# Kernel tuning notes

Hardware: AMD Instinct MI355X
Metric: run time of the kernel (lower is better)

The kernel has to match this reference:

```python
import jax, jax.numpy as jnp
import numpy as np

TAU = 0.1
K = 60.0
CHUNK = 64
B = 1024


def setup_inputs() -> dict:
    key = jax.random.key(0)
    k1, k2, k3, k4 = jax.random.split(key, 4)
    s_v = jax.random.normal(k1, (B, B), jnp.float32)
    s_l = jax.random.normal(k2, (B, B), jnp.float32)
    # class-label based positive/negative masks (typical metric-learning batch)
    labels = jax.random.randint(k3, (B,), 0, B // 8)
    pos_mask = labels[:, None] == labels[None, :]
    neg_mask = ~pos_mask
    w_v = jax.random.uniform(k4, (B, B), jnp.float32)
    w_l = 1.0 - w_v
    return dict(s_v=s_v, s_l=s_l, pos_mask=pos_mask, neg_mask=neg_mask, w_v=w_v, w_l=w_l)


def _soft_ranks(sim, pos_f, neg_f, tau=TAU, chunk=CHUNK):
    """Row-chunked differentiable soft ranks. sim/pos_f/neg_f: [B, B] float."""
    b = sim.shape[0]
    nc = b // chunk  # B divisible by chunk

    def body(args):
        cs, cp, cn = args                                   # [chunk, B] each
        # sig[c, k, j] = sigmoid((s_ck - s_cj) / tau)
        sig = jax.nn.sigmoid((cs[:, :, None] - cs[:, None, :]) / tau)
        rank_pos = 1.0 + jnp.einsum('ckj,ck->cj', sig, cn)  # count negatives above
        rank_neg = 1.0 + jnp.einsum('ckj,ck->cj', sig, cp)  # count positives above
        return rank_pos * cp + rank_neg * cn

    args = (sim.reshape(nc, chunk, b), pos_f.reshape(nc, chunk, b), neg_f.reshape(nc, chunk, b))
    return jax.lax.map(jax.checkpoint(body), args).reshape(b, b)


def reference(s_v, s_l, pos_mask, neg_mask, w_v, w_l):
    pos_f = pos_mask.astype(s_v.dtype)
    neg_f = neg_mask.astype(s_v.dtype)
    rank_v = _soft_ranks(s_v, pos_f, neg_f)
    rank_l = _soft_ranks(s_l, pos_f, neg_f)
    S_hat = (K + 1.0) * (w_v / (K + rank_v) + w_l / (K + rank_l))
    return S_hat
```

## Files before the change

### kernel.cpp

```cpp
#include <hip/hip_runtime.h>


#define NB 1024
#define CEXP 14.426950408889634f
#define SCL  0.000030517578125f
#define NBUK 86
#define BUK0 4.3f
#define BUKW 10.0f
#define DBUK 2
#define CHSZ 128
#define NJOB 32
#define MAXPOS 64

__device__ __forceinline__ float fma_sat(float a, float b, float c) {
    float d;
    asm("v_fma_f32 %0, %1, %2, %3 clamp" : "=v"(d) : "v"(a), "v"(b), "v"(c));
    return d;
}

__device__ __forceinline__ float nrcp(float d) {
    float r = __uint_as_float(0x7EF311C3u - __float_as_uint(d));
    r = r * fmaf(-d, r, 2.0f);
    return r;
}

#define TREE(Es, ra, rb, A)                                      \
    {                                                            \
        const float y1 = fma_sat((Es), (ra).x, SCL);             \
        const float y2 = fma_sat((Es), (ra).y, SCL);             \
        const float y3 = fma_sat((Es), (ra).z, SCL);             \
        const float y4 = fma_sat((Es), (ra).w, SCL);             \
        const float y5 = fma_sat((Es), (rb).x, SCL);             \
        const float y6 = fma_sat((Es), (rb).y, SCL);             \
        const float y7 = fma_sat((Es), (rb).z, SCL);             \
        const float y8 = fma_sat((Es), (rb).w, SCL);             \
        const float p12 = y1 * y2, p34 = y3 * y4;                \
        const float p56 = y5 * y6, p78 = y7 * y8;                \
        const float s12 = y1 + y2, s34 = y3 + y4;                \
        const float s56 = y5 + y6, s78 = y7 + y8;                \
        const float q1 = p12 * p34, q2 = p56 * p78;              \
        const float n1 = fmaf(s12, p34, s34 * p12);              \
        const float n2 = fmaf(s56, p78, s78 * p56);              \
        const float num = fmaf(n1, q2, n2 * q1);                 \
        const float den = q1 * q2;                               \
        (A) = fmaf(num, nrcp(den), (A));                         \
    }

__global__ __launch_bounds__(512) void drank_kernel(
    const float* __restrict__ s_v, const float* __restrict__ s_l,
    const unsigned char* __restrict__ pos_m,
    const unsigned char* __restrict__ neg_m,
    const float* __restrict__ w_v, const float* __restrict__ w_l,
    float* __restrict__ out)
{
    __shared__ float  listRv[NB], listRl[NB];
    __shared__ int    listJv[NB], listJl[NB];
    __shared__ float  sAv1[NB], sAl1[NB];
    __shared__ float  sAv2[NB], sAl2[NB];
    __shared__ int    offv[NBUK + 1], offl[NBUK + 1];
    __shared__ float  SRv[129], SEv[129];
    __shared__ float  SRl[129], SEl[129];
    __shared__ float2 posR[MAXPOS];
    __shared__ int    npos_s, jobCtr;

    int* curv = (int*)sAv1;
    int* curl = (int*)sAl1;

    const int c = blockIdx.x;
    const int t = threadIdx.x;
    const long row = (long)c * NB;

    if (t < NBUK) { curv[t] = 0; curl[t] = 0; }
    if (t == 0) { npos_s = 0; jobCtr = 0; }
    __syncthreads();

    const unsigned int W =
        ((const unsigned int*)pos_m)[0] ^ ((const unsigned int*)neg_m)[0];
    const int mode = (W == 0x01010101u) ? 0 : ((W == 0x3f800000u) ? 2 : 1);

    const int j0 = t * 2;
    const float2 sjv = *(const float2*)(s_v + row + j0);
    const float2 sjl = *(const float2*)(s_l + row + j0);
    const float svu[2] = {sjv.x, sjv.y};
    const float slu[2] = {sjl.x, sjl.y};

    float Rv[2], Rl[2], Ev[2], El[2];
    int ibv[2], ibl[2];
    #pragma unroll
    for (int u = 0; u < 2; ++u) {
        Rv[u] = __builtin_amdgcn_exp2f(-svu[u] * CEXP);
        Rl[u] = __builtin_amdgcn_exp2f(-slu[u] * CEXP);
        Ev[u] = __builtin_amdgcn_exp2f(svu[u] * CEXP);
        El[u] = __builtin_amdgcn_exp2f(slu[u] * CEXP);
        ibv[u] = max(0, min(NBUK - 1, (int)((svu[u] + BUK0) * BUKW)));
        ibl[u] = max(0, min(NBUK - 1, (int)((slu[u] + BUK0) * BUKW)));
        atomicAdd(&curv[ibv[u]], 1);
        atomicAdd(&curl[ibl[u]], 1);
    }

    bool pj[2];
    if (mode == 0) {
        const unsigned short b = ((const unsigned short*)pos_m)[(row >> 1) + t];
        pj[0] = (b & 0x00ffu) != 0; pj[1] = (b & 0xff00u) != 0;
    } else if (mode == 2) {
        const float2 p = *(const float2*)((const float*)pos_m + row + j0);
        pj[0] = p.x != 0.f; pj[1] = p.y != 0.f;
    } else {
        const int2 p = *(const int2*)((const int*)pos_m + row + j0);
        pj[0] = p.x != 0; pj[1] = p.y != 0;
    }
    #pragma unroll
    for (int u = 0; u < 2; ++u) {
        if (pj[u]) {
            const int idx = atomicAdd(&npos_s, 1);
            if (idx < MAXPOS) posR[idx] = make_float2(Rv[u], Rl[u]);
        }
    }
    __syncthreads();

    if (t == 0) {
        int a = 0;
        for (int b = 0; b < NBUK; ++b) { offv[b] = a; a += curv[b]; }
        offv[NBUK] = a;
    }
    if (t == 64) {
        int a = 0;
        for (int b = 0; b < NBUK; ++b) { offl[b] = a; a += curl[b]; }
        offl[NBUK] = a;
    }
    __syncthreads();
    if (t < NBUK) { curv[t] = offv[t]; curl[t] = offl[t]; }
    __syncthreads();

    #pragma unroll
    for (int u = 0; u < 2; ++u) {
        const int pv = atomicAdd(&curv[ibv[u]], 1);
        listRv[pv] = Rv[u];
        listJv[pv] = (j0 + u) | (ibv[u] << 16);
        const int pl = atomicAdd(&curl[ibl[u]], 1);
        listRl[pl] = Rl[u];
        listJl[pl] = (j0 + u) | (ibl[u] << 16);
    }
    __syncthreads();

    if (t < 256) {
        const int m = t >> 7, o = t & 127;
        const float4* L4 = (const float4*)(m ? listRl : listRv);
        const float4 a = L4[2 * o], b = L4[2 * o + 1];
        const float sR = ((a.x + a.y) + (a.z + a.w)) + ((b.x + b.y) + (b.z + b.w));
        const float sE =
            ((__builtin_amdgcn_rcpf(a.x) + __builtin_amdgcn_rcpf(a.y)) +
             (__builtin_amdgcn_rcpf(a.z) + __builtin_amdgcn_rcpf(a.w))) +
            ((__builtin_amdgcn_rcpf(b.x) + __builtin_amdgcn_rcpf(b.y)) +
             (__builtin_amdgcn_rcpf(b.z) + __builtin_amdgcn_rcpf(b.w)));
        (m ? SRl : SRv)[o] = sR;
        (m ? SEl : SEv)[o] = sE;
    }
    __syncthreads();
    if (t == 0)   { float a = 0; SRv[128] = 0;
                    for (int o = 127; o >= 0; --o) { a += SRv[o]; SRv[o] = a; } }
    if (t == 64)  { float a = 0;
                    for (int o = 0; o < 128; ++o) { const float x = SEv[o]; SEv[o] = a; a += x; }
                    SEv[128] = a; }
    if (t == 128) { float a = 0; SRl[128] = 0;
                    for (int o = 127; o >= 0; --o) { a += SRl[o]; SRl[o] = a; } }
    if (t == 192) { float a = 0;
                    for (int o = 0; o < 128; ++o) { const float x = SEl[o]; SEl[o] = a; a += x; }
                    SEl[128] = a; }
    __syncthreads();

    static const unsigned char CORD[8] = {3, 4, 2, 5, 1, 6, 0, 7};
    const int lane = t & 63;

    for (;;) {
        int jid0 = 0;
        if (lane == 0) jid0 = atomicAdd(&jobCtr, 1);
        const int jid = __builtin_amdgcn_readfirstlane(jid0);
        if (jid >= NJOB) break;
        const int ch = CORD[jid >> 2];
        const int m  = (jid >> 1) & 1;
        const int h  = jid & 1;

        const float*  LR  = m ? listRl : listRv;
        const int*    LJ  = m ? listJl : listJv;
        const int*    off = m ? offl : offv;
        float*        SA  = h ? (m ? sAl2 : sAv2) : (m ? sAl1 : sAv1);
        const float*  SR  = m ? SRl : SRv;
        const float*  SE  = m ? SEl : SEv;
        const float4* L4  = (const float4*)LR;

        const int p0 = ch * CHSZ + 2 * lane;
        const float2 R2 = *(const float2*)(LR + p0);
        const int2   jj = *(const int2*)(LJ + p0);
        const float Ex = __builtin_amdgcn_rcpf(R2.x);
        const float Ey = __builtin_amdgcn_rcpf(R2.y);
        const float EsX = SCL * Ex;
        const float EsY = SCL * Ey;

        const int bs = LJ[ch * CHSZ] >> 16;
        const int be = LJ[ch * CHSZ + CHSZ - 1] >> 16;
        const int lo0 = off[max(0, bs - DBUK)] & ~7;
        const int hi0 = (off[min(NBUK - 1, be + DBUK) + 1] + 7) & ~7;
        const int mid = ((lo0 + hi0) >> 1) & ~7;
        const int lo = h ? mid : lo0;
        const int hi = h ? hi0 : mid;

        float a0 = 0.f, a1 = 0.f;
        #pragma unroll 2
        for (int p = lo; p < hi; p += 8) {
            const float4 ra = L4[p >> 2];
            const float4 rb = L4[(p >> 2) + 1];
            TREE(EsX, ra, rb, a0);
            TREE(EsY, ra, rb, a1);
        }
        float cx, cy;
        if (h) {
            const float sr = SR[hi0 >> 3];
            cx = fmaf(-Ex, sr, (float)(NB - hi0));
            cy = fmaf(-Ey, sr, (float)(NB - hi0));
        } else {
            const float se = SE[lo0 >> 3];
            cx = R2.x * se;
            cy = R2.y * se;
        }
        SA[jj.x & 0xFFFF] = fmaf(a0, SCL, cx);
        SA[jj.y & 0xFFFF] = fmaf(a1, SCL, cy);
    }

    float sPv[2] = {0.f, 0.f};
    float sPl[2] = {0.f, 0.f};
    const int np = min(npos_s, MAXPOS);
    for (int i = 0; i < np; ++i) {
        const float2 rp = posR[i];
        #pragma unroll
        for (int u = 0; u < 2; ++u) {
            sPv[u] += __builtin_amdgcn_rcpf(fmaf(Ev[u], rp.x, 1.0f));
            sPl[u] += __builtin_amdgcn_rcpf(fmaf(El[u], rp.y, 1.0f));
        }
    }
    __syncthreads();

    const float2 av1 = *(const float2*)(sAv1 + j0);
    const float2 av2 = *(const float2*)(sAv2 + j0);
    const float2 al1 = *(const float2*)(sAl1 + j0);
    const float2 al2 = *(const float2*)(sAl2 + j0);
    const float sAvu[2] = {av1.x + av2.x, av1.y + av2.y};
    const float sAlu[2] = {al1.x + al2.x, al1.y + al2.y};
    const float2 wv = *(const float2*)(w_v + row + j0);
    const float2 wl = *(const float2*)(w_l + row + j0);
    const float wva[2] = {wv.x, wv.y};
    const float wla[2] = {wl.x, wl.y};
    float o[2];
    #pragma unroll
    for (int u = 0; u < 2; ++u) {
        const float rv = pj[u] ? (1.0f + sAvu[u] - sPv[u]) : (1.0f + sPv[u]);
        const float rl = pj[u] ? (1.0f + sAlu[u] - sPl[u]) : (1.0f + sPl[u]);
        o[u] = 61.0f * (wva[u] / (60.0f + rv) + wla[u] / (60.0f + rl));
    }
    float2 o2;
    o2.x = o[0]; o2.y = o[1];
    *(float2*)(out + row + j0) = o2;
}

extern "C" void kernel_launch(void* const* d_in, const int* in_sizes, int n_in,
                              void* d_out, int out_size, void* d_ws, size_t ws_size,
                              hipStream_t stream) {
    const float* s_v = (const float*)d_in[0];
    const float* s_l = (const float*)d_in[1];
    const unsigned char* pos_m = (const unsigned char*)d_in[2];
    const unsigned char* neg_m = (const unsigned char*)d_in[3];
    const float* w_v = (const float*)d_in[4];
    const float* w_l = (const float*)d_in[5];
    float* out = (float*)d_out;

    drank_kernel<<<dim3(NB), dim3(512), 0, stream>>>(s_v, s_l, pos_m, neg_m, w_v, w_l, out);
}
```

Measured before the change: 124.9 us.

## Add second-order tail corrections so fewer exact sigmoid neighbours are needed

```diff
diff --git a/kernel.cpp b/kernel.cpp
--- a/kernel.cpp
+++ b/kernel.cpp
@@ -4,13 +4,14 @@
 #define NB 1024
 #define CEXP 14.426950408889634f
 #define SCL  0.000030517578125f
-#define NBUK 86
+#define NBUK 128
 #define BUK0 4.3f
-#define BUKW 10.0f
+#define BUKW 14.883720930f
 #define DBUK 2
 #define CHSZ 128
 #define NJOB 32
 #define MAXPOS 64
+#define ECLMP 1e17f
 
 __device__ __forceinline__ float fma_sat(float a, float b, float c) {
     float d;
@@ -59,7 +60,9 @@
     __shared__ float  sAv2[NB], sAl2[NB];
     __shared__ int    offv[NBUK + 1], offl[NBUK + 1];
     __shared__ float  SRv[129], SEv[129];
+    __shared__ float  SR2v[129], SE2v[129];
     __shared__ float  SRl[129], SEl[129];
+    __shared__ float  SR2l[129], SE2l[129];
     __shared__ float2 posR[MAXPOS];
     __shared__ int    npos_s, jobCtr;
 
@@ -147,14 +150,24 @@
         const int m = t >> 7, o = t & 127;
         const float4* L4 = (const float4*)(m ? listRl : listRv);
         const float4 a = L4[2 * o], b = L4[2 * o + 1];
-        const float sR = ((a.x + a.y) + (a.z + a.w)) + ((b.x + b.y) + (b.z + b.w));
-        const float sE =
-            ((__builtin_amdgcn_rcpf(a.x) + __builtin_amdgcn_rcpf(a.y)) +
-             (__builtin_amdgcn_rcpf(a.z) + __builtin_amdgcn_rcpf(a.w))) +
-            ((__builtin_amdgcn_rcpf(b.x) + __builtin_amdgcn_rcpf(b.y)) +
-             (__builtin_amdgcn_rcpf(b.z) + __builtin_amdgcn_rcpf(b.w)));
-        (m ? SRl : SRv)[o] = sR;
-        (m ? SEl : SEv)[o] = sE;
+        const float r1 = fminf(a.x, ECLMP), r2 = fminf(a.y, ECLMP);
+        const float r3 = fminf(a.z, ECLMP), r4 = fminf(a.w, ECLMP);
+        const float r5 = fminf(b.x, ECLMP), r6 = fminf(b.y, ECLMP);
+        const float r7 = fminf(b.z, ECLMP), r8 = fminf(b.w, ECLMP);
+        const float e1 = fminf(__builtin_amdgcn_rcpf(a.x), ECLMP);
+        const float e2 = fminf(__builtin_amdgcn_rcpf(a.y), ECLMP);
+        const float e3 = fminf(__builtin_amdgcn_rcpf(a.z), ECLMP);
+        const float e4 = fminf(__builtin_amdgcn_rcpf(a.w), ECLMP);
+        const float e5 = fminf(__builtin_amdgcn_rcpf(b.x), ECLMP);
+        const float e6 = fminf(__builtin_amdgcn_rcpf(b.y), ECLMP);
+        const float e7 = fminf(__builtin_amdgcn_rcpf(b.z), ECLMP);
+        const float e8 = fminf(__builtin_amdgcn_rcpf(b.w), ECLMP);
+        (m ? SRl  : SRv )[o] = ((r1 + r2) + (r3 + r4)) + ((r5 + r6) + (r7 + r8));
+        (m ? SEl  : SEv )[o] = ((e1 + e2) + (e3 + e4)) + ((e5 + e6) + (e7 + e8));
+        (m ? SR2l : SR2v)[o] = ((r1*r1 + r2*r2) + (r3*r3 + r4*r4)) +
+                               ((r5*r5 + r6*r6) + (r7*r7 + r8*r8));
+        (m ? SE2l : SE2v)[o] = ((e1*e1 + e2*e2) + (e3*e3 + e4*e4)) +
+                               ((e5*e5 + e6*e6) + (e7*e7 + e8*e8));
     }
     __syncthreads();
     if (t == 0)   { float a = 0; SRv[128] = 0;
@@ -167,6 +180,16 @@
     if (t == 192) { float a = 0;
                     for (int o = 0; o < 128; ++o) { const float x = SEl[o]; SEl[o] = a; a += x; }
                     SEl[128] = a; }
+    if (t == 256) { float a = 0; SR2v[128] = 0;
+                    for (int o = 127; o >= 0; --o) { a += SR2v[o]; SR2v[o] = a; } }
+    if (t == 320) { float a = 0;
+                    for (int o = 0; o < 128; ++o) { const float x = SE2v[o]; SE2v[o] = a; a += x; }
+                    SE2v[128] = a; }
+    if (t == 384) { float a = 0; SR2l[128] = 0;
+                    for (int o = 127; o >= 0; --o) { a += SR2l[o]; SR2l[o] = a; } }
+    if (t == 448) { float a = 0;
+                    for (int o = 0; o < 128; ++o) { const float x = SE2l[o]; SE2l[o] = a; a += x; }
+                    SE2l[128] = a; }
     __syncthreads();
 
     static const unsigned char CORD[8] = {3, 4, 2, 5, 1, 6, 0, 7};
@@ -187,6 +210,8 @@
         float*        SA  = h ? (m ? sAl2 : sAv2) : (m ? sAl1 : sAv1);
         const float*  SR  = m ? SRl : SRv;
         const float*  SE  = m ? SEl : SEv;
+        const float*  SR2 = m ? SR2l : SR2v;
+        const float*  SE2 = m ? SE2l : SE2v;
         const float4* L4  = (const float4*)LR;
 
         const int p0 = ch * CHSZ + 2 * lane;
@@ -215,13 +240,14 @@
         }
         float cx, cy;
         if (h) {
-            const float sr = SR[hi0 >> 3];
-            cx = fmaf(-Ex, sr, (float)(NB - hi0));
-            cy = fmaf(-Ey, sr, (float)(NB - hi0));
+            const float sr = SR[hi0 >> 3], sr2 = SR2[hi0 >> 3];
+            const float Exc = fminf(Ex, ECLMP), Eyc = fminf(Ey, ECLMP);
+            cx = (float)(NB - hi0) - Exc * sr + (Exc * Exc) * sr2;
+            cy = (float)(NB - hi0) - Eyc * sr + (Eyc * Eyc) * sr2;
         } else {
-            const float se = SE[lo0 >> 3];
-            cx = R2.x * se;
-            cy = R2.y * se;
+            const float se = SE[lo0 >> 3], se2 = SE2[lo0 >> 3];
+            cx = R2.x * se - (R2.x * R2.x) * se2;
+            cy = R2.y * se - (R2.y * R2.y) * se2;
         }
         SA[jj.x & 0xFFFF] = fmaf(a0, SCL, cx);
         SA[jj.y & 0xFFFF] = fmaf(a1, SCL, cy);
```

New measurement: 120.6 us. -3.4%, faster.
